# Performance work log

Measured on AMD Instinct MI355X. Metric: run time of the kernel, lower is better.

The kernel has to match this reference:

```python
import jax, jax.numpy as jnp
import numpy as np

RADIUS = 2
P = 8 * RADIUS  # n_points = 16
PAD = RADIUS + 1

# Circular sample offsets, matching skimage local_binary_pattern:
#   rp = -R*sin(2*pi*i/P), cp = R*cos(2*pi*i/P), rounded to 8 decimals.
_ang = 2.0 * np.pi * np.arange(P) / P
_RP = np.round(-RADIUS * np.sin(_ang), 8)
_CP = np.round(RADIUS * np.cos(_ang), 8)


def lbp_var(img):
    """LBP 'var' transform: per-pixel population variance of the P
    bilinearly-interpolated circular neighbors (zero padding outside).
    img: [B, C, H, W] -> [B, C, H, W]
    """
    B, C, H, W = img.shape
    padded = jnp.pad(img, ((0, 0), (0, 0), (PAD, PAD), (PAD, PAD)))

    def shifted(dr, dc):
        # static-offset slice of the padded image == image sampled at (r+dr, c+dc)
        return padded[:, :, PAD + dr:PAD + dr + H, PAD + dc:PAD + dc + W]

    s1 = jnp.zeros_like(img)
    s2 = jnp.zeros_like(img)
    for i in range(P):  # small fixed loop over the 16 circle points
        rp, cp = float(_RP[i]), float(_CP[i])
        fr, fc = int(np.floor(rp)), int(np.floor(cp))
        tr, tc = rp - fr, cp - fc
        v = jnp.zeros_like(img)
        for (dr, dc, w) in ((fr, fc, (1 - tr) * (1 - tc)),
                            (fr, fc + 1, (1 - tr) * tc),
                            (fr + 1, fc, tr * (1 - tc)),
                            (fr + 1, fc + 1, tr * tc)):
            if w > 1e-12:  # skip exactly-zero bilinear weights (static)
                v = v + jnp.float32(w) * shifted(dr, dc)
        s1 = s1 + v
        s2 = s2 + v * v
    mean = s1 / P
    var = s2 / P - mean * mean
    return jnp.nan_to_num(var)


def reference(output, target):
    out_lbp = lbp_var(output)
    trg_lbp = lbp_var(target)
    return jnp.mean((out_lbp - trg_lbp) ** 2)


def setup_inputs() -> dict:
    key = jax.random.key(0)
    k1, k2 = jax.random.split(key)
    shape = (16, 3, 512, 512)
    return {
        "output": jax.random.uniform(k1, shape, dtype=jnp.float32),
        "target": jax.random.uniform(k2, shape, dtype=jnp.float32),
    }
```

## Files before the change

### kernel.cpp

```cpp
#include <hip/hip_runtime.h>

#define IMG_H 512
#define IMG_W 512
#define TILE_X 64
#define TILE_Y 16
#define LDS_H  20
#define LDS_COLS 68
#define LDS_W  72
#define NBLOCKS ((IMG_W / TILE_X) * (IMG_H / TILE_Y) * 48)

constexpr double RPV[16] = {
   0.0,        -0.76536686, -1.41421356, -1.84775907,
  -2.0,        -1.84775907, -1.41421356, -0.76536686,
   0.0,         0.76536686,  1.41421356,  1.84775907,
   2.0,         1.84775907,  1.41421356,  0.76536686
};
constexpr double CPV[16] = {
   2.0,         1.84775907,  1.41421356,  0.76536686,
   0.0,        -0.76536686, -1.41421356, -1.84775907,
  -2.0,        -1.84775907, -1.41421356, -0.76536686,
   0.0,         0.76536686,  1.41421356,  1.84775907
};

constexpr int cfloor(double x) {
  int i = (int)x;
  return (x < (double)i) ? i - 1 : i;
}

template<int I>
__device__ __forceinline__ void lbp_point(const float (&w)[5][8], int px,
                                          float& s1, float& s2) {
  constexpr double rp = RPV[I], cp = CPV[I];
  constexpr int fr = cfloor(rp), fc = cfloor(cp);
  constexpr double tr = rp - (double)fr, tc = cp - (double)fc;
  constexpr double w00 = (1.0 - tr) * (1.0 - tc);
  constexpr double w01 = (1.0 - tr) * tc;
  constexpr double w10 = tr * (1.0 - tc);
  constexpr double w11 = tr * tc;
  float v = 0.0f;
  if constexpr (w00 > 1e-12) v += (float)w00 * w[fr + 2][px + fc + 2];
  if constexpr (w01 > 1e-12) v += (float)w01 * w[fr + 2][px + fc + 3];
  if constexpr (w10 > 1e-12) v += (float)w10 * w[fr + 3][px + fc + 2];
  if constexpr (w11 > 1e-12) v += (float)w11 * w[fr + 3][px + fc + 3];
  s1 += v;
  s2 += v * v;
}

__device__ __forceinline__ void lbp_all16(const float (&w)[5][8], int px,
                                          float& s1, float& s2) {
  lbp_point<0>(w, px, s1, s2);  lbp_point<1>(w, px, s1, s2);
  lbp_point<2>(w, px, s1, s2);  lbp_point<3>(w, px, s1, s2);
  lbp_point<4>(w, px, s1, s2);  lbp_point<5>(w, px, s1, s2);
  lbp_point<6>(w, px, s1, s2);  lbp_point<7>(w, px, s1, s2);
  lbp_point<8>(w, px, s1, s2);  lbp_point<9>(w, px, s1, s2);
  lbp_point<10>(w, px, s1, s2); lbp_point<11>(w, px, s1, s2);
  lbp_point<12>(w, px, s1, s2); lbp_point<13>(w, px, s1, s2);
  lbp_point<14>(w, px, s1, s2); lbp_point<15>(w, px, s1, s2);
}

__global__ __launch_bounds__(256)
void lbp_loss_kernel(const float* __restrict__ A, const float* __restrict__ B,
                     double* __restrict__ part) {
  __shared__ __align__(16) float tile[2][LDS_H][LDS_W];
  __shared__ double bsum[4];

  const int tid = threadIdx.x;
  const int bx = blockIdx.x, by = blockIdx.y, z = blockIdx.z;
  const int row0 = by * TILE_Y - 2;
  const int col0 = bx * TILE_X - 2;
  const size_t ibase = (size_t)z * (IMG_H * IMG_W);

  const int PAIRS = LDS_COLS / 2;
  const int PER_IMG = LDS_H * PAIRS;
  for (int idx = tid; idx < 2 * PER_IMG; idx += 256) {
    const int im = idx >= PER_IMG;
    const int k = im ? idx - PER_IMG : idx;
    const int r = k / PAIRS;
    const int pc = k - r * PAIRS;
    const int gr = row0 + r;
    const int gc = col0 + pc * 2;
    float2 v = make_float2(0.0f, 0.0f);
    if ((unsigned)gr < (unsigned)IMG_H && (unsigned)gc < (unsigned)(IMG_W - 1)) {
      const float* __restrict__ src = im ? B : A;
      v = *(const float2*)&src[ibase + (size_t)gr * IMG_W + gc];
    }
    tile[im][r][pc * 2]     = v.x;
    tile[im][r][pc * 2 + 1] = v.y;
  }
  __syncthreads();

  const int tx = tid & 15;
  const int ty = tid >> 4;

  float var2[2][4];
  #pragma unroll
  for (int im = 0; im < 2; ++im) {
    float w[5][8];
    #pragma unroll
    for (int r = 0; r < 5; ++r) {
      float4 a = *(const float4*)&tile[im][ty + r][tx * 4];
      float4 b = *(const float4*)&tile[im][ty + r][tx * 4 + 4];
      w[r][0] = a.x; w[r][1] = a.y; w[r][2] = a.z; w[r][3] = a.w;
      w[r][4] = b.x; w[r][5] = b.y; w[r][6] = b.z; w[r][7] = b.w;
    }
    #pragma unroll
    for (int px = 0; px < 4; ++px) {
      float s1 = 0.0f, s2 = 0.0f;
      lbp_all16(w, px, s1, s2);
      float mean = s1 * 0.0625f;
      var2[im][px] = s2 * 0.0625f - mean * mean;
    }
  }

  float local = 0.0f;
  #pragma unroll
  for (int px = 0; px < 4; ++px) {
    float d = var2[0][px] - var2[1][px];
    local += d * d;
  }

  #pragma unroll
  for (int off = 32; off > 0; off >>= 1)
    local += __shfl_down(local, off, 64);
  if ((tid & 63) == 0) bsum[tid >> 6] = (double)local;
  __syncthreads();
  if (tid == 0) {
    const int bflat = bx + gridDim.x * (by + gridDim.y * z);
    part[bflat] = bsum[0] + bsum[1] + bsum[2] + bsum[3];
  }
}

__global__ __launch_bounds__(1024)
void reduce_kernel(const double* __restrict__ part, int n,
                   float* __restrict__ out, double inv_n) {
  __shared__ double sm[16];
  double s = 0.0;
  for (int i = threadIdx.x; i < n; i += 1024) s += part[i];
  #pragma unroll
  for (int off = 32; off > 0; off >>= 1)
    s += __shfl_down(s, off, 64);
  if ((threadIdx.x & 63) == 0) sm[threadIdx.x >> 6] = s;
  __syncthreads();
  if (threadIdx.x < 16) {
    double t = sm[threadIdx.x];
    #pragma unroll
    for (int off = 8; off > 0; off >>= 1)
      t += __shfl_down(t, off, 64);
    if (threadIdx.x == 0) out[0] = (float)(t * inv_n);
  }
}

extern "C" void kernel_launch(void* const* d_in, const int* in_sizes, int n_in,
                              void* d_out, int out_size, void* d_ws, size_t ws_size,
                              hipStream_t stream) {
  const float* A = (const float*)d_in[0];
  const float* B = (const float*)d_in[1];
  float* out = (float*)d_out;
  double* part = (double*)d_ws;

  const int total = in_sizes[0];
  const int BC = total / (IMG_H * IMG_W);
  dim3 grid(IMG_W / TILE_X, IMG_H / TILE_Y, BC);
  lbp_loss_kernel<<<grid, 256, 0, stream>>>(A, B, part);

  const int nblocks = grid.x * grid.y * grid.z;
  reduce_kernel<<<1, 1024, 0, stream>>>(part, nblocks, out, 1.0 / (double)total);
}
```

Before: 161.3 us.

## Interleave A/B images in LDS and compute both with packed float2 FMAs

Stores the two input images interleaved as float2 pairs in shared memory and processes them together using two-wide vector FMA operations, which can map to packed FP32 instructions. Global loads switch to float4 for both images in one loop, with the halo widened to keep loads 16-byte aligned. This is meant to halve the VALU instruction count for the bilinear stencil and simplify the load loop, at the cost of a larger LDS tile and possible extra register pressure.

```diff
diff --git a/kernel.cpp b/kernel.cpp
--- a/kernel.cpp
+++ b/kernel.cpp
@@ -1,13 +1,15 @@
 #include <hip/hip_runtime.h>
+
+
+typedef float f2 __attribute__((ext_vector_type(2)));
 
 #define IMG_H 512
 #define IMG_W 512
 #define TILE_X 64
 #define TILE_Y 16
 #define LDS_H  20
-#define LDS_COLS 68
-#define LDS_W  72
-#define NBLOCKS ((IMG_W / TILE_X) * (IMG_H / TILE_Y) * 48)
+#define LDS_CP 72
+#define LDS_SP 74
 
 constexpr double RPV[16] = {
    0.0,        -0.76536686, -1.41421356, -1.84775907,
@@ -27,27 +29,33 @@
   return (x < (double)i) ? i - 1 : i;
 }
 
+__device__ __forceinline__ f2 splat(float x) { f2 r; r.x = x; r.y = x; return r; }
+
 template<int I>
-__device__ __forceinline__ void lbp_point(const float (&w)[5][8], int px,
-                                          float& s1, float& s2) {
+__device__ __forceinline__ void lbp_point(const f2 (&w)[5][8], int px,
+                                          f2& s1, f2& s2) {
   constexpr double rp = RPV[I], cp = CPV[I];
   constexpr int fr = cfloor(rp), fc = cfloor(cp);
   constexpr double tr = rp - (double)fr, tc = cp - (double)fc;
-  constexpr double w00 = (1.0 - tr) * (1.0 - tc);
-  constexpr double w01 = (1.0 - tr) * tc;
-  constexpr double w10 = tr * (1.0 - tc);
-  constexpr double w11 = tr * tc;
-  float v = 0.0f;
-  if constexpr (w00 > 1e-12) v += (float)w00 * w[fr + 2][px + fc + 2];
-  if constexpr (w01 > 1e-12) v += (float)w01 * w[fr + 2][px + fc + 3];
-  if constexpr (w10 > 1e-12) v += (float)w10 * w[fr + 3][px + fc + 2];
-  if constexpr (w11 > 1e-12) v += (float)w11 * w[fr + 3][px + fc + 3];
-  s1 += v;
-  s2 += v * v;
+  constexpr double W00 = (1.0 - tr) * (1.0 - tc);
+  constexpr double W01 = (1.0 - tr) * tc;
+  constexpr double W10 = tr * (1.0 - tc);
+  constexpr double W11 = tr * tc;
+  f2 v = splat(0.0f);
+  if constexpr (W00 > 1e-12)
+    v = __builtin_elementwise_fma(splat((float)W00), w[fr + 2][px + fc + 2], v);
+  if constexpr (W01 > 1e-12)
+    v = __builtin_elementwise_fma(splat((float)W01), w[fr + 2][px + fc + 3], v);
+  if constexpr (W10 > 1e-12)
+    v = __builtin_elementwise_fma(splat((float)W10), w[fr + 3][px + fc + 2], v);
+  if constexpr (W11 > 1e-12)
+    v = __builtin_elementwise_fma(splat((float)W11), w[fr + 3][px + fc + 3], v);
+  s1 = s1 + v;
+  s2 = __builtin_elementwise_fma(v, v, s2);
 }
 
-__device__ __forceinline__ void lbp_all16(const float (&w)[5][8], int px,
-                                          float& s1, float& s2) {
+__device__ __forceinline__ void lbp_all16(const f2 (&w)[5][8], int px,
+                                          f2& s1, f2& s2) {
   lbp_point<0>(w, px, s1, s2);  lbp_point<1>(w, px, s1, s2);
   lbp_point<2>(w, px, s1, s2);  lbp_point<3>(w, px, s1, s2);
   lbp_point<4>(w, px, s1, s2);  lbp_point<5>(w, px, s1, s2);
@@ -61,62 +69,63 @@
 __global__ __launch_bounds__(256)
 void lbp_loss_kernel(const float* __restrict__ A, const float* __restrict__ B,
                      double* __restrict__ part) {
-  __shared__ __align__(16) float tile[2][LDS_H][LDS_W];
+  __shared__ __align__(16) f2 tile[LDS_H][LDS_SP];
   __shared__ double bsum[4];
 
   const int tid = threadIdx.x;
   const int bx = blockIdx.x, by = blockIdx.y, z = blockIdx.z;
   const int row0 = by * TILE_Y - 2;
-  const int col0 = bx * TILE_X - 2;
+  const int col0 = bx * TILE_X - 4;
   const size_t ibase = (size_t)z * (IMG_H * IMG_W);
 
-  const int PAIRS = LDS_COLS / 2;
-  const int PER_IMG = LDS_H * PAIRS;
-  for (int idx = tid; idx < 2 * PER_IMG; idx += 256) {
-    const int im = idx >= PER_IMG;
-    const int k = im ? idx - PER_IMG : idx;
-    const int r = k / PAIRS;
-    const int pc = k - r * PAIRS;
+  const int QUADS = LDS_CP / 4;
+  const int SLOTS = LDS_H * QUADS;
+  for (int idx = tid; idx < SLOTS; idx += 256) {
+    const int r = idx / QUADS;
+    const int q = idx - r * QUADS;
     const int gr = row0 + r;
-    const int gc = col0 + pc * 2;
-    float2 v = make_float2(0.0f, 0.0f);
-    if ((unsigned)gr < (unsigned)IMG_H && (unsigned)gc < (unsigned)(IMG_W - 1)) {
-      const float* __restrict__ src = im ? B : A;
-      v = *(const float2*)&src[ibase + (size_t)gr * IMG_W + gc];
+    const int gc = col0 + q * 4;
+    float4 a = make_float4(0.f, 0.f, 0.f, 0.f);
+    float4 b = make_float4(0.f, 0.f, 0.f, 0.f);
+    if ((unsigned)gr < (unsigned)IMG_H && (unsigned)gc < (unsigned)IMG_W) {
+      const size_t off = ibase + (size_t)gr * IMG_W + gc;
+      a = *(const float4*)&A[off];
+      b = *(const float4*)&B[off];
     }
-    tile[im][r][pc * 2]     = v.x;
-    tile[im][r][pc * 2 + 1] = v.y;
+    f2* dst = &tile[r][q * 4];
+    dst[0] = f2{a.x, b.x};
+    dst[1] = f2{a.y, b.y};
+    dst[2] = f2{a.z, b.z};
+    dst[3] = f2{a.w, b.w};
   }
   __syncthreads();
 
   const int tx = tid & 15;
   const int ty = tid >> 4;
 
-  float var2[2][4];
+  f2 w[5][8];
   #pragma unroll
-  for (int im = 0; im < 2; ++im) {
-    float w[5][8];
-    #pragma unroll
-    for (int r = 0; r < 5; ++r) {
-      float4 a = *(const float4*)&tile[im][ty + r][tx * 4];
-      float4 b = *(const float4*)&tile[im][ty + r][tx * 4 + 4];
-      w[r][0] = a.x; w[r][1] = a.y; w[r][2] = a.z; w[r][3] = a.w;
-      w[r][4] = b.x; w[r][5] = b.y; w[r][6] = b.z; w[r][7] = b.w;
-    }
-    #pragma unroll
-    for (int px = 0; px < 4; ++px) {
-      float s1 = 0.0f, s2 = 0.0f;
-      lbp_all16(w, px, s1, s2);
-      float mean = s1 * 0.0625f;
-      var2[im][px] = s2 * 0.0625f - mean * mean;
-    }
+  for (int r = 0; r < 5; ++r) {
+    const f2* lp = &tile[ty + r][tx * 4 + 2];
+    float4 q0 = *(const float4*)(lp + 0);
+    float4 q1 = *(const float4*)(lp + 2);
+    float4 q2 = *(const float4*)(lp + 4);
+    float4 q3 = *(const float4*)(lp + 6);
+    w[r][0] = f2{q0.x, q0.y}; w[r][1] = f2{q0.z, q0.w};
+    w[r][2] = f2{q1.x, q1.y}; w[r][3] = f2{q1.z, q1.w};
+    w[r][4] = f2{q2.x, q2.y}; w[r][5] = f2{q2.z, q2.w};
+    w[r][6] = f2{q3.x, q3.y}; w[r][7] = f2{q3.z, q3.w};
   }
 
   float local = 0.0f;
   #pragma unroll
   for (int px = 0; px < 4; ++px) {
-    float d = var2[0][px] - var2[1][px];
-    local += d * d;
+    f2 s1 = splat(0.0f), s2 = splat(0.0f);
+    lbp_all16(w, px, s1, s2);
+    f2 mean = s1 * 0.0625f;
+    f2 var  = __builtin_elementwise_fma(-mean, mean, s2 * 0.0625f);
+    const float d = var.x - var.y;
+    local = fmaf(d, d, local);
   }
 
   #pragma unroll
```

Measured after the change: 143.3 us. 11.1% less time.
